# Kernel tuning notes

Measured on AMD Instinct MI355X. Metric: run time of the kernel, lower is better.

The kernel has to match this reference:

```python
import jax, jax.numpy as jnp
import numpy as np

N_NODES = 100000
N_EDGES = 3200000
D_FEAT = 64


def setup_inputs() -> dict:
    key = jax.random.key(0)
    k1, k2, k3 = jax.random.split(key, 3)
    inputs = jax.random.normal(k1, (N_NODES, D_FEAT), dtype=jnp.float32)
    rows = jax.random.randint(k2, (N_EDGES,), 0, N_NODES, dtype=jnp.int32)
    cols = jax.random.randint(k3, (N_EDGES,), 0, N_NODES, dtype=jnp.int32)
    return {"inputs": inputs, "rows": rows, "cols": cols}


def reference(inputs, rows, cols):
    # adj is a binary sparse [N, N] matrix given as COO edges (rows[e], cols[e]) -> 1.0
    n = inputs.shape[0]
    # degrees = adj.sum(dim=1): count of outgoing edges per row
    deg = jax.ops.segment_sum(jnp.ones_like(rows, dtype=inputs.dtype), rows,
                              num_segments=n)  # [N]
    # degrees + (degrees == 0): avoid div-by-zero for isolated nodes
    deg = deg + (deg == 0).astype(inputs.dtype)
    # spmm(adj, inputs): sum neighbor features into each row
    agg = jax.ops.segment_sum(inputs[cols], rows, num_segments=n)  # [N, d]
    return agg / deg[:, None]
```

## Files before the change

### kernel.cpp

```cpp
#include <hip/hip_runtime.h>
#include <hip/hip_bf16.h>
#include <hip/hip_fp16.h>

#define D_FEAT 64
#define TILE_EDGES 8192
#define SC_THREADS 512
#define ROWS_PER_BUK 128
#define BUK_SHIFT 7
#define STRIDE 4480

__global__ void __launch_bounds__(SC_THREADS) scatter_kernel(
    const float* __restrict__ x, __half* __restrict__ x16,
    const int* __restrict__ rows, const int* __restrict__ cols,
    int* __restrict__ gcount, int* __restrict__ ebuf,
    int n_edges, int nbuk, int n4)
{
    __shared__ int lh[1024];
    __shared__ int lscan[1024];
    __shared__ int lgb[1024];
    __shared__ int lsort[TILE_EDGES];

    const int t = threadIdx.x;

    {
        const int per = (n4 + gridDim.x - 1) / gridDim.x;
        const int s0 = blockIdx.x * per;
        const int e0 = min(s0 + per, n4);
        for (int i = s0 + t; i < e0; i += SC_THREADS) {
            float4 v = ((const float4*)x)[i];
            ushort4 u;
            u.x = __half_as_ushort(__float2half(v.x));
            u.y = __half_as_ushort(__float2half(v.y));
            u.z = __half_as_ushort(__float2half(v.z));
            u.w = __half_as_ushort(__float2half(v.w));
            ((ushort4*)x16)[i] = u;
        }
    }

    lh[t] = 0; lh[t + 512] = 0;
    __syncthreads();

    const int tb = blockIdx.x * TILE_EDGES;
    const int te = min(tb + TILE_EDGES, n_edges);

    for (int e = tb + t * 4; e < te; e += SC_THREADS * 4) {
        if (e + 4 <= te) {
            int4 r4 = *(const int4*)&rows[e];
            atomicAdd(&lh[r4.x >> BUK_SHIFT], 1);
            atomicAdd(&lh[r4.y >> BUK_SHIFT], 1);
            atomicAdd(&lh[r4.z >> BUK_SHIFT], 1);
            atomicAdd(&lh[r4.w >> BUK_SHIFT], 1);
        } else {
            for (int k = e; k < te; ++k) atomicAdd(&lh[rows[k] >> BUK_SHIFT], 1);
        }
    }
    __syncthreads();

    const int c0 = lh[2 * t], c1 = lh[2 * t + 1];
    const int s2 = c0 + c1;
    lscan[t] = s2;
    __syncthreads();
    for (int ofs = 1; ofs < 512; ofs <<= 1) {
        int val = lscan[t];
        int add = (t >= ofs) ? lscan[t - ofs] : 0;
        __syncthreads();
        lscan[t] = val + add;
        __syncthreads();
    }
    const int excl = lscan[t] - s2;
    __syncthreads();
    lscan[2 * t] = excl;
    lscan[2 * t + 1] = excl + c0;
    lgb[2 * t]     = c0 ? atomicAdd(&gcount[2 * t], c0) : 0;
    lgb[2 * t + 1] = c1 ? atomicAdd(&gcount[2 * t + 1], c1) : 0;
    lh[2 * t] = excl;
    lh[2 * t + 1] = excl + c0;
    __syncthreads();

    for (int e = tb + t * 4; e < te; e += SC_THREADS * 4) {
        if (e + 4 <= te) {
            int4 r4 = *(const int4*)&rows[e];
            int4 c4 = *(const int4*)&cols[e];
            int p0 = atomicAdd(&lh[r4.x >> BUK_SHIFT], 1);
            int p1 = atomicAdd(&lh[r4.y >> BUK_SHIFT], 1);
            int p2 = atomicAdd(&lh[r4.z >> BUK_SHIFT], 1);
            int p3 = atomicAdd(&lh[r4.w >> BUK_SHIFT], 1);
            lsort[p0] = ((r4.x & (ROWS_PER_BUK - 1)) << 17) | c4.x;
            lsort[p1] = ((r4.y & (ROWS_PER_BUK - 1)) << 17) | c4.y;
            lsort[p2] = ((r4.z & (ROWS_PER_BUK - 1)) << 17) | c4.z;
            lsort[p3] = ((r4.w & (ROWS_PER_BUK - 1)) << 17) | c4.w;
        } else {
            for (int k = e; k < te; ++k) {
                int r = rows[k], c = cols[k];
                int pos = atomicAdd(&lh[r >> BUK_SHIFT], 1);
                lsort[pos] = ((r & (ROWS_PER_BUK - 1)) << 17) | c;
            }
        }
    }
    __syncthreads();

    const int hw = t >> 5;
    const int hl = t & 31;
    for (int b = hw; b < nbuk; b += 16) {
        const int ls = lscan[b];
        const int cnt = lh[b] - ls;
        const int gb = lgb[b];
        for (int i = hl; i < cnt; i += 32) {
            int gpos = gb + i;
            if (gpos < STRIDE) ebuf[b * STRIDE + gpos] = lsort[ls + i];
        }
    }
}

__global__ void __launch_bounds__(512) gather_kernel(
    const uint4* __restrict__ x4, const int* __restrict__ gcount,
    const int* __restrict__ ebuf, float* __restrict__ out, int n_nodes)
{
    __shared__ int lcol[STRIDE];
    __shared__ int lh[ROWS_PER_BUK];
    __shared__ int lscan[ROWS_PER_BUK];
    __shared__ int lcur[ROWS_PER_BUK];
    const int b = blockIdx.x;
    const int t = threadIdx.x;

    const int start = b * STRIDE;
    int cnt = gcount[b];
    if (cnt > STRIDE) cnt = STRIDE;

    if (t < ROWS_PER_BUK) lh[t] = 0;
    __syncthreads();
    for (int i = t; i < cnt; i += 512) atomicAdd(&lh[ebuf[start + i] >> 17], 1);
    __syncthreads();

    int v0 = (t < ROWS_PER_BUK) ? lh[t] : 0;
    if (t < ROWS_PER_BUK) lscan[t] = v0;
    __syncthreads();
    for (int ofs = 1; ofs < ROWS_PER_BUK; ofs <<= 1) {
        int val = 0;
        if (t < ROWS_PER_BUK) {
            val = lscan[t];
            if (t >= ofs) val += lscan[t - ofs];
        }
        __syncthreads();
        if (t < ROWS_PER_BUK) lscan[t] = val;
        __syncthreads();
    }
    if (t < ROWS_PER_BUK) {
        int excl = lscan[t] - v0;
        lscan[t] = excl;
        lcur[t] = excl;
    }
    __syncthreads();

    for (int i = t; i < cnt; i += 512) {
        int p = ebuf[start + i];
        int pos = atomicAdd(&lcur[p >> 17], 1);
        lcol[pos] = p & 0x1FFFF;
    }
    __syncthreads();

    const int w = t >> 6;
    const int lane = t & 63;
    const int eg = lane >> 3;
    const int g2 = lane & 7;

    union U { uint4 u; __half2 h2[4]; };

    for (int rr = 0; rr < 16; ++rr) {
        const int r = w * 16 + rr;
        const int row = (b << BUK_SHIFT) + r;
        const int s = lscan[r];
        const int d = lh[r];
        const int e = s + d;

        const __half2 z = __float2half2_rn(0.0f);
        __half2 h[4];
        #pragma unroll
        for (int k = 0; k < 4; ++k) h[k] = z;

        int j = s;
        for (; j + 32 <= e; j += 32) {
            int cA = lcol[j + eg], cB = lcol[j + 8 + eg];
            int cC = lcol[j + 16 + eg], cD = lcol[j + 24 + eg];
            U A, B, C, D;
            A.u = x4[cA * 8 + g2];
            B.u = x4[cB * 8 + g2];
            C.u = x4[cC * 8 + g2];
            D.u = x4[cD * 8 + g2];
            #pragma unroll
            for (int k = 0; k < 4; ++k)
                h[k] = __hadd2(h[k], __hadd2(__hadd2(A.h2[k], B.h2[k]),
                                             __hadd2(C.h2[k], D.h2[k])));
        }
        for (; j + 16 <= e; j += 16) {
            int cA = lcol[j + eg], cB = lcol[j + 8 + eg];
            U A, B;
            A.u = x4[cA * 8 + g2];
            B.u = x4[cB * 8 + g2];
            #pragma unroll
            for (int k = 0; k < 4; ++k)
                h[k] = __hadd2(h[k], __hadd2(A.h2[k], B.h2[k]));
        }
        for (; j + 8 <= e; j += 8) {
            int c = lcol[j + eg];
            U A;
            A.u = x4[c * 8 + g2];
            #pragma unroll
            for (int k = 0; k < 4; ++k) h[k] = __hadd2(h[k], A.h2[k]);
        }
        int rem = e - j;
        if (eg < rem) {
            int c = lcol[j + eg];
            U A;
            A.u = x4[c * 8 + g2];
            #pragma unroll
            for (int k = 0; k < 4; ++k) h[k] = __hadd2(h[k], A.h2[k]);
        }

        float a[8];
        #pragma unroll
        for (int k = 0; k < 4; ++k) {
            float2 f = __half22float2(h[k]);
            a[2 * k] = f.x;
            a[2 * k + 1] = f.y;
        }
        #pragma unroll
        for (int k = 0; k < 8; ++k) {
            a[k] += __shfl_down(a[k], 8, 64);
            a[k] += __shfl_down(a[k], 16, 64);
            a[k] += __shfl_down(a[k], 32, 64);
        }

        if (eg == 0 && row < n_nodes) {
            const float inv = 1.0f / (float)(d > 0 ? d : 1);
            float4* o = (float4*)(out + ((long)row << 6) + (g2 << 3));
            o[0] = make_float4(a[0] * inv, a[1] * inv, a[2] * inv, a[3] * inv);
            o[1] = make_float4(a[4] * inv, a[5] * inv, a[6] * inv, a[7] * inv);
        }
    }
}

extern "C" void kernel_launch(void* const* d_in, const int* in_sizes, int n_in,
                              void* d_out, int out_size, void* d_ws, size_t ws_size,
                              hipStream_t stream) {
    const float* x  = (const float*)d_in[0];
    const int* rows = (const int*)d_in[1];
    const int* cols = (const int*)d_in[2];
    float* out = (float*)d_out;

    const int n_nodes = in_sizes[0] / D_FEAT;
    const int n_edges = in_sizes[1];
    const int n_feat_total = in_sizes[0];
    const int n4 = n_feat_total / 4;

    const int nbuk   = (n_nodes + ROWS_PER_BUK - 1) >> BUK_SHIFT;
    const int ntiles = (n_edges + TILE_EDGES - 1) / TILE_EDGES;

    __half* x16 = (__half*)d_ws;
    int* gcount = (int*)(x16 + n_feat_total);
    int* ebuf   = gcount + nbuk;

    hipMemsetAsync(gcount, 0, (size_t)nbuk * sizeof(int), stream);

    scatter_kernel<<<ntiles, SC_THREADS, 0, stream>>>(
        x, x16, rows, cols, gcount, ebuf, n_edges, nbuk, n4);

    gather_kernel<<<nbuk, 512, 0, stream>>>((const uint4*)x16, gcount, ebuf, out, n_nodes);
}
```

Measured before the change: 182.7 us.

## Replace barrier-heavy LDS scans with wavefront shuffle scans and enlarge edge tiles

Both block-wide prefix scans, the 512-wide bucket scan in the scatter kernel and the 128-wide row scan in the gather kernel, now use 64-lane __shfl_up wavefront scans plus a small per-wave sum table. This removes many __syncthreads rounds. The edge tile grows from 8192 to 12500 edges, so there are fewer scatter blocks and fewer global atomic reservations per bucket, at the cost of more LDS per block and lower occupancy. The bucket flush now assigns 16 lanes per bucket instead of 32, which shortens the per-bucket loops.

```diff
diff --git a/kernel.cpp b/kernel.cpp
--- a/kernel.cpp
+++ b/kernel.cpp
@@ -1,9 +1,8 @@
 #include <hip/hip_runtime.h>
-#include <hip/hip_bf16.h>
 #include <hip/hip_fp16.h>
 
 #define D_FEAT 64
-#define TILE_EDGES 8192
+#define TILE_EDGES 12500
 #define SC_THREADS 512
 #define ROWS_PER_BUK 128
 #define BUK_SHIFT 7
@@ -19,8 +18,11 @@
     __shared__ int lscan[1024];
     __shared__ int lgb[1024];
     __shared__ int lsort[TILE_EDGES];
+    __shared__ int wsum[8];
 
     const int t = threadIdx.x;
+    const int w = t >> 6;
+    const int lane = t & 63;
 
     {
         const int per = (n4 + gridDim.x - 1) / gridDim.x;
@@ -58,23 +60,26 @@
 
     const int c0 = lh[2 * t], c1 = lh[2 * t + 1];
     const int s2 = c0 + c1;
-    lscan[t] = s2;
-    __syncthreads();
-    for (int ofs = 1; ofs < 512; ofs <<= 1) {
-        int val = lscan[t];
-        int add = (t >= ofs) ? lscan[t - ofs] : 0;
+    {
+        int val = s2;
+        #pragma unroll
+        for (int ofs = 1; ofs < 64; ofs <<= 1) {
+            int n = __shfl_up(val, ofs, 64);
+            if (lane >= ofs) val += n;
+        }
+        if (lane == 63) wsum[w] = val;
         __syncthreads();
-        lscan[t] = val + add;
-        __syncthreads();
-    }
-    const int excl = lscan[t] - s2;
-    __syncthreads();
-    lscan[2 * t] = excl;
-    lscan[2 * t + 1] = excl + c0;
-    lgb[2 * t]     = c0 ? atomicAdd(&gcount[2 * t], c0) : 0;
-    lgb[2 * t + 1] = c1 ? atomicAdd(&gcount[2 * t + 1], c1) : 0;
-    lh[2 * t] = excl;
-    lh[2 * t + 1] = excl + c0;
+        int off = 0;
+        #pragma unroll
+        for (int k = 0; k < 8; ++k) off += (k < w) ? wsum[k] : 0;
+        const int excl = off + val - s2;
+        lscan[2 * t] = excl;
+        lscan[2 * t + 1] = excl + c0;
+        lgb[2 * t]     = c0 ? atomicAdd(&gcount[2 * t], c0) : 0;
+        lgb[2 * t + 1] = c1 ? atomicAdd(&gcount[2 * t + 1], c1) : 0;
+        lh[2 * t] = excl;
+        lh[2 * t + 1] = excl + c0;
+    }
     __syncthreads();
 
     for (int e = tb + t * 4; e < te; e += SC_THREADS * 4) {
@@ -99,13 +104,13 @@
     }
     __syncthreads();
 
-    const int hw = t >> 5;
-    const int hl = t & 31;
-    for (int b = hw; b < nbuk; b += 16) {
+    const int qw = t >> 4;
+    const int ql = t & 15;
+    for (int b = qw; b < nbuk; b += 32) {
         const int ls = lscan[b];
         const int cnt = lh[b] - ls;
         const int gb = lgb[b];
-        for (int i = hl; i < cnt; i += 32) {
+        for (int i = ql; i < cnt; i += 16) {
             int gpos = gb + i;
             if (gpos < STRIDE) ebuf[b * STRIDE + gpos] = lsort[ls + i];
         }
@@ -132,23 +137,20 @@
     for (int i = t; i < cnt; i += 512) atomicAdd(&lh[ebuf[start + i] >> 17], 1);
     __syncthreads();
 
-    int v0 = (t < ROWS_PER_BUK) ? lh[t] : 0;
-    if (t < ROWS_PER_BUK) lscan[t] = v0;
-    __syncthreads();
-    for (int ofs = 1; ofs < ROWS_PER_BUK; ofs <<= 1) {
-        int val = 0;
-        if (t < ROWS_PER_BUK) {
-            val = lscan[t];
-            if (t >= ofs) val += lscan[t - ofs];
-        }
-        __syncthreads();
-        if (t < ROWS_PER_BUK) lscan[t] = val;
-        __syncthreads();
-    }
-    if (t < ROWS_PER_BUK) {
-        int excl = lscan[t] - v0;
-        lscan[t] = excl;
-        lcur[t] = excl;
+    if (t < 64) {
+        int cA = lh[2 * t], cB = lh[2 * t + 1];
+        int s2 = cA + cB;
+        int val = s2;
+        #pragma unroll
+        for (int ofs = 1; ofs < 64; ofs <<= 1) {
+            int n = __shfl_up(val, ofs, 64);
+            if (t >= ofs) val += n;
+        }
+        int excl = val - s2;
+        lscan[2 * t] = excl;
+        lscan[2 * t + 1] = excl + cA;
+        lcur[2 * t] = excl;
+        lcur[2 * t + 1] = excl + cA;
     }
     __syncthreads();
 
```

Measured after the change: 176.6 us. 3.4% less time.
